# Performance work log

Measured on AMD Instinct MI355X. Metric: run time of the kernel, lower is better.

Reference implementation:

```python
import jax, jax.numpy as jnp
import numpy as np

N, E, F_IN, NUM_GRAPHS, K = 50000, 500000, 160, 128, 3


def _glorot(k, shape):
    lim = np.sqrt(6.0 / (shape[-2] + shape[-1])).astype(np.float32)
    return jax.random.uniform(k, shape, jnp.float32, -lim, lim)


def setup_inputs() -> dict:
    key = jax.random.key(0)
    ks = jax.random.split(key, 8)
    x = jax.random.normal(ks[0], (N, F_IN), jnp.float32)
    edge_index = jax.random.randint(ks[1], (2, E), 0, N)
    edge_attr = jax.random.uniform(ks[2], (E,), jnp.float32)
    batch = jnp.sort(jax.random.randint(ks[3], (N,), 0, NUM_GRAPHS))
    W1 = _glorot(ks[4], (K, F_IN, 128)); b1 = jnp.zeros((128,), jnp.float32)
    W2 = _glorot(ks[5], (K, 128, 64)); b2 = jnp.zeros((64,), jnp.float32)
    W3 = _glorot(ks[6], (K, 64, 32)); b3 = jnp.zeros((32,), jnp.float32)
    Wl = _glorot(ks[7], (32, 2)); bl = jnp.zeros((2,), jnp.float32)
    return dict(x=x, edge_index=edge_index, edge_attr=edge_attr, batch=batch,
                W1=W1, b1=b1, W2=W2, b2=b2, W3=W3, b3=b3, Wl=Wl, bl=bl)


def _cheb_norm(src, dst, edge_attr, n):
    # PyG ChebConv: sym-normalized Laplacian, lambda_max=2 =>
    # L_hat = (2/lmax)*L_sym - I = -D^{-1/2} A D^{-1/2} (diagonal = 0)
    deg = jax.ops.segment_sum(edge_attr, src, num_segments=n)
    safe = jnp.where(deg > 0, deg, 1.0)
    dinv = jnp.where(deg > 0, jax.lax.rsqrt(safe), 0.0)
    return -dinv[src] * edge_attr * dinv[dst]


def _propagate(x, src, dst, w, n):
    # out[dst] += w * x[src]  (sparse L_hat @ x)
    return jax.ops.segment_sum(w[:, None] * x[src], dst, num_segments=n)


def _cheb_conv(x, src, dst, w, W, b, n):
    # Chebyshev recurrence: T0 = x, T1 = L_hat x, Tk = 2 L_hat T(k-1) - T(k-2)
    tx0 = x
    out = tx0 @ W[0]
    tx1 = _propagate(tx0, src, dst, w, n)
    out = out + tx1 @ W[1]
    for k in range(2, W.shape[0]):
        tx2 = 2.0 * _propagate(tx1, src, dst, w, n) - tx0
        out = out + tx2 @ W[k]
        tx0, tx1 = tx1, tx2
    return out + b


def reference(x, edge_index, edge_attr, batch, W1, b1, W2, b2, W3, b3, Wl, bl):
    n = x.shape[0]
    src, dst = edge_index[0], edge_index[1]
    w = _cheb_norm(src, dst, edge_attr, n)
    h = jax.nn.relu(_cheb_conv(x, src, dst, w, W1, b1, n))
    h = jax.nn.relu(_cheb_conv(h, src, dst, w, W2, b2, n))
    h = jax.nn.relu(_cheb_conv(h, src, dst, w, W3, b3, n))
    # global_mean_pool over graph ids (dropout omitted: eval mode)
    sums = jax.ops.segment_sum(h, batch, num_segments=NUM_GRAPHS)
    cnt = jax.ops.segment_sum(jnp.ones((n,), h.dtype), batch, num_segments=NUM_GRAPHS)
    pooled = sums / jnp.maximum(cnt, 1.0)[:, None]
    return pooled @ Wl + bl
```

## Files before the change

kernel.cpp:

```cpp
#include <hip/hip_runtime.h>

#define N_NODES 50000
#define N_EDGES 500000
#define NUM_G   128
#define SCAN_NB 49
#define PN      (SCAN_NB * 1024)
#define HIST_NCX 64
#define HIST_EC  7813
#define HIST_R   16384
#define HIST_NRY 4

typedef __attribute__((ext_vector_type(8))) short short8;
typedef __attribute__((ext_vector_type(4))) float f32x4;

__device__ __forceinline__ unsigned f2bf(float x) {
    unsigned u = __float_as_uint(x);
    return (u + 0x7FFFu + ((u >> 16) & 1u)) >> 16;
}
__device__ __forceinline__ float bf2f(unsigned h) {
    return __uint_as_float(h << 16);
}

__global__ void hist_kernel(const int* __restrict__ src, const int* __restrict__ dst,
                            const float* __restrict__ ea,
                            float* __restrict__ pdeg, int* __restrict__ pcnt) {
    __shared__ unsigned lh[HIST_R];
    int x = blockIdx.x, y = blockIdx.y, tid = threadIdx.x;
    bool isdeg = y < HIST_NRY;
    int base = (isdeg ? y : y - HIST_NRY) * HIST_R;
    for (int i = tid; i < HIST_R; i += 256) lh[i] = 0u;
    __syncthreads();
    int e0 = x * HIST_EC, e1 = min(e0 + HIST_EC, N_EDGES);
    if (isdeg) {
        for (int e = e0 + tid; e < e1; e += 256) {
            int s = src[e];
            if ((unsigned)(s - base) < HIST_R) atomicAdd((float*)&lh[s - base], ea[e]);
        }
    } else {
        for (int e = e0 + tid; e < e1; e += 256) {
            int d = dst[e];
            if ((unsigned)(d - base) < HIST_R) atomicAdd((int*)&lh[d - base], 1);
        }
    }
    __syncthreads();
    if (isdeg) {
        for (int i = tid; i < HIST_R; i += 256) {
            int n = base + i;
            if (n < PN) pdeg[(size_t)x * PN + n] = ((float*)lh)[i];
        }
    } else {
        for (int i = tid; i < HIST_R; i += 256) {
            int n = base + i;
            if (n < PN) pcnt[(size_t)x * PN + n] = ((int*)lh)[i];
        }
    }
}

__global__ void reduce_kernel(const float* __restrict__ pdeg, int* __restrict__ pcnt,
                              float* __restrict__ dinv, int* __restrict__ cnt) {
    int n = blockIdx.x * 256 + threadIdx.x;
    float d = 0.f;
    int run = 0;
    for (int x = 0; x < HIST_NCX; ++x) {
        d += pdeg[(size_t)x * PN + n];
        int v = pcnt[(size_t)x * PN + n];
        pcnt[(size_t)x * PN + n] = run;
        run += v;
    }
    if (n < N_NODES) {
        float r = 0.f;
        if (d > 0.f) {
            r = rsqrtf(d);
            r = r * (1.5f - 0.5f * d * r * r);
        }
        dinv[n] = r;
        cnt[n] = run;
    } else {
        cnt[n] = 0;
    }
}

__global__ void scan_partial_kernel(const int* __restrict__ cnt, int* __restrict__ partial) {
    int b = blockIdx.x, t = threadIdx.x;
    int4 v = reinterpret_cast<const int4*>(cnt)[b * 256 + t];
    int s = v.x + v.y + v.z + v.w;
    __shared__ int red[256];
    red[t] = s;
    __syncthreads();
    for (int off = 128; off > 0; off >>= 1) {
        if (t < off) red[t] += red[t + off];
        __syncthreads();
    }
    if (t == 0) partial[b] = red[0];
}

__global__ void scan_offsets_kernel(int* __restrict__ partial, int* __restrict__ rowptr,
                                    int nb, int n) {
    int t = threadIdx.x;
    int orig = (t < nb) ? partial[t] : 0;
    int v = orig;
    for (int off = 1; off < 64; off <<= 1) {
        int u = __shfl_up(v, off, 64);
        if (t >= off) v += u;
    }
    if (t < nb) partial[t] = v - orig;
    if (t == nb - 1) rowptr[n] = v;
}

__global__ void scan_final_kernel(const int* __restrict__ cnt, const int* __restrict__ partial,
                                  int* __restrict__ rowptr, int n) {
    int b = blockIdx.x, t = threadIdx.x;
    int4 v = reinterpret_cast<const int4*>(cnt)[b * 256 + t];
    int s = v.x + v.y + v.z + v.w;
    __shared__ int red[256];
    red[t] = s;
    __syncthreads();
    for (int off = 1; off < 256; off <<= 1) {
        int u = (t >= off) ? red[t - off] : 0;
        __syncthreads();
        red[t] += u;
        __syncthreads();
    }
    int excl = partial[b] + ((t == 0) ? 0 : red[t - 1]);
    int i0 = b * 1024 + t * 4;
    if (i0 < n)     rowptr[i0]     = excl;
    if (i0 + 1 < n) rowptr[i0 + 1] = excl + v.x;
    if (i0 + 2 < n) rowptr[i0 + 2] = excl + v.x + v.y;
    if (i0 + 3 < n) rowptr[i0 + 3] = excl + v.x + v.y + v.z;
}

__global__ void scatter_kernel(const int* __restrict__ src, const int* __restrict__ dst,
                               const float* __restrict__ ea,
                               const int* __restrict__ rowptr, const int* __restrict__ pcnt,
                               int2* __restrict__ csr) {
    __shared__ int cursor[HIST_R];
    int x = blockIdx.x, y = blockIdx.y, tid = threadIdx.x;
    int base = y * HIST_R;
    for (int i = tid; i < HIST_R; i += 256) {
        int n = base + i;
        cursor[i] = (n < N_NODES) ? (rowptr[n] + pcnt[(size_t)x * PN + n]) : 0;
    }
    __syncthreads();
    int e0 = x * HIST_EC, e1 = min(e0 + HIST_EC, N_EDGES);
    for (int e = e0 + tid; e < e1; e += 256) {
        int d = dst[e];
        if ((unsigned)(d - base) < HIST_R) {
            int pos = atomicAdd(&cursor[d - base], 1);
            int2 ew;
            ew.x = src[e];
            ew.y = __float_as_int(ea[e]);
            csr[pos] = ew;
        }
    }
}

__global__ void conv_bf16_kernel(const float* __restrict__ x, unsigned short* __restrict__ o, int n4) {
    int t = blockIdx.x * blockDim.x + threadIdx.x;
    if (t >= n4) return;
    float4 v = reinterpret_cast<const float4*>(x)[t];
    ushort4 r;
    r.x = (unsigned short)f2bf(v.x);
    r.y = (unsigned short)f2bf(v.y);
    r.z = (unsigned short)f2bf(v.z);
    r.w = (unsigned short)f2bf(v.w);
    *reinterpret_cast<ushort4*>(o + (size_t)t * 4) = r;
}

__device__ __forceinline__ void wprep_one(const float* __restrict__ W, unsigned short* __restrict__ WT,
                                          int t, int FIN, int F) {
    int n = t / FIN, k = t - n * FIN;
    int sel = n / F, c = n - sel * F;
    float v;
    if (sel == 0) v = W[(size_t)k * F + c] - W[(size_t)2 * FIN * F + (size_t)k * F + c];
    else          v = W[(size_t)sel * FIN * F + (size_t)k * F + c];
    WT[t] = (unsigned short)f2bf(v);
}

__global__ void wprep_all_kernel(const float* __restrict__ W1, const float* __restrict__ W2,
                                 const float* __restrict__ W3,
                                 unsigned short* __restrict__ WT1, unsigned short* __restrict__ WT2,
                                 unsigned short* __restrict__ WT3) {
    int t = blockIdx.x * 256 + threadIdx.x;
    if (t < 61440)      wprep_one(W1, WT1, t, 160, 128);
    else if (t < 86016) wprep_one(W2, WT2, t - 61440, 128, 64);
    else if (t < 92160) wprep_one(W3, WT3, t - 86016, 64, 32);
}

template<int FIN, int F>
__launch_bounds__(256)
__global__ void cheb_gemm(const unsigned short* __restrict__ Xb, const unsigned short* __restrict__ WT,
                          const float* __restrict__ dinv,
                          unsigned short* __restrict__ Y0, unsigned short* __restrict__ Y1,
                          unsigned short* __restrict__ Y2,
                          int nrows) {
    constexpr int KT = FIN / 32;
    constexpr int NT = F / 32;
    constexpr int SA = FIN + 8;
    constexpr int F8 = FIN / 8;
    __shared__ short Bs[32 * SA];

    int tid = threadIdx.x;
    int lane = tid & 63, w = tid >> 6;
    int m0 = blockIdx.x * 64;
    int g = blockIdx.y;
    unsigned short* Ys = (g == 0) ? Y0 : (g == 1) ? Y1 : Y2;

    int colb = lane & 15;
    int q8 = (lane >> 4) << 3;
    int rq = (lane >> 4) << 2;
    int arow = m0 + w * 16 + colb;
    bool rok = arow < nrows;

    short8 afr[KT];
    #pragma unroll
    for (int kt = 0; kt < KT; ++kt) {
        short8 z = {0, 0, 0, 0, 0, 0, 0, 0};
        afr[kt] = rok ? *reinterpret_cast<const short8*>(Xb + (size_t)arow * FIN + (kt << 5) + q8) : z;
    }

    for (int nt = 0; nt < NT; ++nt) {
        int n0 = (g * NT + nt) << 5;
        __syncthreads();
        for (int span = tid; span < 32 * F8; span += 256) {
            int r = span / F8, c8 = (span - r * F8) << 3;
            int pr = (r < 16) ? (r << 1) : (((r - 16) << 1) + 1);
            *reinterpret_cast<uint4*>(&Bs[r * SA + c8]) =
                *reinterpret_cast<const uint4*>(WT + (size_t)(n0 + pr) * FIN + c8);
        }
        __syncthreads();

        f32x4 acc0 = {0.f, 0.f, 0.f, 0.f}, acc1 = acc0;
        #pragma unroll
        for (int kt = 0; kt < KT; ++kt) {
            short8 b0 = *reinterpret_cast<const short8*>(&Bs[colb * SA + (kt << 5) + q8]);
            short8 b1 = *reinterpret_cast<const short8*>(&Bs[(colb + 16) * SA + (kt << 5) + q8]);
            acc0 = __builtin_amdgcn_mfma_f32_16x16x32_bf16(afr[kt], b0, acc0, 0, 0, 0);
            acc1 = __builtin_amdgcn_mfma_f32_16x16x32_bf16(afr[kt], b1, acc1, 0, 0, 0);
        }

        int lc = (nt << 5) + (colb << 1);
        #pragma unroll
        for (int r = 0; r < 4; ++r) {
            int orow = m0 + w * 16 + rq + r;
            if (orow < nrows) {
                float sc = (g == 2) ? dinv[orow] : 1.0f;
                unsigned pack = f2bf(acc0[r] * sc) | (f2bf(acc1[r] * sc) << 16);
                *reinterpret_cast<unsigned*>(Ys + (size_t)orow * F + lc) = pack;
            }
        }
    }
}

__device__ __forceinline__ void acc8(float* acc, uint4 p, float wv) {
    acc[0] += wv * bf2f(p.x & 0xFFFFu);
    acc[1] += wv * __uint_as_float(p.x & 0xFFFF0000u);
    acc[2] += wv * bf2f(p.y & 0xFFFFu);
    acc[3] += wv * __uint_as_float(p.y & 0xFFFF0000u);
    acc[4] += wv * bf2f(p.z & 0xFFFFu);
    acc[5] += wv * __uint_as_float(p.z & 0xFFFF0000u);
    acc[6] += wv * bf2f(p.w & 0xFFFFu);
    acc[7] += wv * __uint_as_float(p.w & 0xFFFF0000u);
}

__device__ __forceinline__ void expand8(uint4 p, float* o) {
    o[0] = bf2f(p.x & 0xFFFFu);
    o[1] = __uint_as_float(p.x & 0xFFFF0000u);
    o[2] = bf2f(p.y & 0xFFFFu);
    o[3] = __uint_as_float(p.y & 0xFFFF0000u);
    o[4] = bf2f(p.z & 0xFFFFu);
    o[5] = __uint_as_float(p.z & 0xFFFF0000u);
    o[6] = bf2f(p.w & 0xFFFFu);
    o[7] = __uint_as_float(p.w & 0xFFFF0000u);
}

__global__ void gather_z_kernel(const unsigned short* __restrict__ X, const int2* __restrict__ csr,
                                const int* __restrict__ rowptr, const float* __restrict__ dinv,
                                const unsigned short* __restrict__ Y1, unsigned short* __restrict__ U,
                                int n, int F) {
    int Fq8 = F >> 3;
    int t = blockIdx.x * blockDim.x + threadIdx.x;
    int d = t / Fq8;
    if (d >= n) return;
    int f8 = (t - d * Fq8) << 3;
    int beg = rowptr[d], end = rowptr[d + 1];
    float acc[8] = {0.f, 0.f, 0.f, 0.f, 0.f, 0.f, 0.f, 0.f};
    int i = beg;
    for (; i + 1 < end; i += 2) {
        int2 e0 = csr[i], e1 = csr[i + 1];
        uint4 p0 = *reinterpret_cast<const uint4*>(X + (size_t)e0.x * F + f8);
        uint4 p1 = *reinterpret_cast<const uint4*>(X + (size_t)e1.x * F + f8);
        acc8(acc, p0, __int_as_float(e0.y));
        acc8(acc, p1, __int_as_float(e1.y));
    }
    if (i < end) {
        int2 e0 = csr[i];
        uint4 p0 = *reinterpret_cast<const uint4*>(X + (size_t)e0.x * F + f8);
        acc8(acc, p0, __int_as_float(e0.y));
    }
    float y[8];
    expand8(*reinterpret_cast<const uint4*>(Y1 + (size_t)d * F + f8), y);
    float dv = dinv[d];
    float dv2 = 2.f * dv;
    uint4 o;
    o.x = f2bf(dv * (y[0] - dv2 * acc[0])) | (f2bf(dv * (y[1] - dv2 * acc[1])) << 16);
    o.y = f2bf(dv * (y[2] - dv2 * acc[2])) | (f2bf(dv * (y[3] - dv2 * acc[3])) << 16);
    o.z = f2bf(dv * (y[4] - dv2 * acc[4])) | (f2bf(dv * (y[5] - dv2 * acc[5])) << 16);
    o.w = f2bf(dv * (y[6] - dv2 * acc[6])) | (f2bf(dv * (y[7] - dv2 * acc[7])) << 16);
    *reinterpret_cast<uint4*>(U + (size_t)d * F + f8) = o;
}

__global__ void gather_v_kernel(const unsigned short* __restrict__ X, const int2* __restrict__ csr,
                                const int* __restrict__ rowptr, const float* __restrict__ dinv,
                                const unsigned short* __restrict__ Y0, const float* __restrict__ bias,
                                unsigned short* __restrict__ Xn, int n, int F) {
    int Fq8 = F >> 3;
    int t = blockIdx.x * blockDim.x + threadIdx.x;
    int d = t / Fq8;
    if (d >= n) return;
    int f8 = (t - d * Fq8) << 3;
    int beg = rowptr[d], end = rowptr[d + 1];
    float acc[8] = {0.f, 0.f, 0.f, 0.f, 0.f, 0.f, 0.f, 0.f};
    int i = beg;
    for (; i + 1 < end; i += 2) {
        int2 e0 = csr[i], e1 = csr[i + 1];
        uint4 p0 = *reinterpret_cast<const uint4*>(X + (size_t)e0.x * F + f8);
        uint4 p1 = *reinterpret_cast<const uint4*>(X + (size_t)e1.x * F + f8);
        acc8(acc, p0, __int_as_float(e0.y));
        acc8(acc, p1, __int_as_float(e1.y));
    }
    if (i < end) {
        int2 e0 = csr[i];
        uint4 p0 = *reinterpret_cast<const uint4*>(X + (size_t)e0.x * F + f8);
        acc8(acc, p0, __int_as_float(e0.y));
    }
    float y[8];
    expand8(*reinterpret_cast<const uint4*>(Y0 + (size_t)d * F + f8), y);
    float4 ba = *reinterpret_cast<const float4*>(bias + f8);
    float4 bb = *reinterpret_cast<const float4*>(bias + f8 + 4);
    float dv = dinv[d];
    float v0 = fmaxf(y[0] - dv * acc[0] + ba.x, 0.f);
    float v1 = fmaxf(y[1] - dv * acc[1] + ba.y, 0.f);
    float v2 = fmaxf(y[2] - dv * acc[2] + ba.z, 0.f);
    float v3 = fmaxf(y[3] - dv * acc[3] + ba.w, 0.f);
    float v4 = fmaxf(y[4] - dv * acc[4] + bb.x, 0.f);
    float v5 = fmaxf(y[5] - dv * acc[5] + bb.y, 0.f);
    float v6 = fmaxf(y[6] - dv * acc[6] + bb.z, 0.f);
    float v7 = fmaxf(y[7] - dv * acc[7] + bb.w, 0.f);
    uint4 o;
    o.x = f2bf(v0) | (f2bf(v1) << 16);
    o.y = f2bf(v2) | (f2bf(v3) << 16);
    o.z = f2bf(v4) | (f2bf(v5) << 16);
    o.w = f2bf(v6) | (f2bf(v7) << 16);
    *reinterpret_cast<uint4*>(Xn + (size_t)d * F + f8) = o;
}

__device__ __forceinline__ int lower_bound_dev(const int* __restrict__ a, int n, int v) {
    int lo = 0, hi = n;
    while (lo < hi) {
        int mid = (lo + hi) >> 1;
        if (a[mid] < v) lo = mid + 1; else hi = mid;
    }
    return lo;
}

__global__ void pool_kernel(const unsigned short* __restrict__ H, const int* __restrict__ batch,
                            const float* __restrict__ Wl, const float* __restrict__ bl,
                            float* __restrict__ out, int n) {
    int g = blockIdx.x;
    int start = lower_bound_dev(batch, n, g);
    int end   = lower_bound_dev(batch, n, g + 1);
    int tid = threadIdx.x;
    int f = tid & 31;
    int sub = tid >> 5;
    float acc = 0.0f;
    for (int i = start + sub; i < end; i += 8)
        acc += bf2f((unsigned)H[(size_t)i * 32 + f]);
    __shared__ float red[256];
    red[tid] = acc;
    __syncthreads();
    if (tid < 128) red[tid] += red[tid + 128];
    __syncthreads();
    if (tid < 64) red[tid] += red[tid + 64];
    __syncthreads();
    if (tid < 32) red[tid] += red[tid + 32];
    __syncthreads();
    if (tid < 2) {
        int cnt = end - start;
        float inv = 1.0f / (float)(cnt > 0 ? cnt : 1);
        float o = bl[tid];
        for (int f2 = 0; f2 < 32; ++f2)
            o += red[f2] * inv * Wl[f2 * 2 + tid];
        out[g * 2 + tid] = o;
    }
}

extern "C" void kernel_launch(void* const* d_in, const int* in_sizes, int n_in,
                              void* d_out, int out_size, void* d_ws, size_t ws_size,
                              hipStream_t stream) {
    const float* x     = (const float*)d_in[0];
    const int*   ei    = (const int*)d_in[1];
    const float* ea    = (const float*)d_in[2];
    const int*   batch = (const int*)d_in[3];
    const float* W1 = (const float*)d_in[4];
    const float* b1 = (const float*)d_in[5];
    const float* W2 = (const float*)d_in[6];
    const float* b2 = (const float*)d_in[7];
    const float* W3 = (const float*)d_in[8];
    const float* b3 = (const float*)d_in[9];
    const float* Wl = (const float*)d_in[10];
    const float* bl = (const float*)d_in[11];
    float* out = (float*)d_out;
    char* ws = (char*)d_ws;

    const int* src = ei;
    const int* dst = ei + N_EDGES;

    size_t off = 0;
    auto alloc = [&](size_t bytes) { char* p = ws + off; off += (bytes + 255) & ~(size_t)255; return p; };
    float* pdeg    = (float*)alloc((size_t)HIST_NCX * PN * 4);
    int*   pcnt    = (int*)  alloc((size_t)HIST_NCX * PN * 4);
    float* dinv    = (float*)alloc(N_NODES * 4);
    int*   cnt     = (int*)  alloc((size_t)PN * 4);
    int*   partial = (int*)  alloc(SCAN_NB * 4);
    int*   rowptr  = (int*)  alloc((N_NODES + 1) * 4);
    int2*  csr     = (int2*) alloc((size_t)N_EDGES * 8);
    unsigned short* Xb  = (unsigned short*)alloc((size_t)N_NODES * 160 * 2);
    unsigned short* Y0  = (unsigned short*)alloc((size_t)N_NODES * 128 * 2);
    unsigned short* Y1  = (unsigned short*)alloc((size_t)N_NODES * 128 * 2);
    unsigned short* Y2  = (unsigned short*)alloc((size_t)N_NODES * 128 * 2);
    unsigned short* U   = (unsigned short*)alloc((size_t)N_NODES * 128 * 2);
    unsigned short* WT1 = (unsigned short*)alloc((size_t)384 * 160 * 2);
    unsigned short* WT2 = (unsigned short*)alloc((size_t)192 * 128 * 2);
    unsigned short* WT3 = (unsigned short*)alloc((size_t)96 * 64 * 2);

    const int BT = 256;

    hist_kernel<<<dim3(HIST_NCX, 2 * HIST_NRY), BT, 0, stream>>>(src, dst, ea, pdeg, pcnt);
    reduce_kernel<<<PN / BT, BT, 0, stream>>>(pdeg, pcnt, dinv, cnt);
    scan_partial_kernel<<<SCAN_NB, BT, 0, stream>>>(cnt, partial);
    scan_offsets_kernel<<<1, 64, 0, stream>>>(partial, rowptr, SCAN_NB, N_NODES);
    scan_final_kernel<<<SCAN_NB, BT, 0, stream>>>(cnt, partial, rowptr, N_NODES);
    scatter_kernel<<<dim3(HIST_NCX, HIST_NRY), BT, 0, stream>>>(src, dst, ea, rowptr, pcnt, csr);

    int n4 = N_NODES * 160 / 4;
    conv_bf16_kernel<<<(n4 + BT - 1) / BT, BT, 0, stream>>>(x, Xb, n4);
    wprep_all_kernel<<<360, BT, 0, stream>>>(W1, W2, W3, WT1, WT2, WT3);

    dim3 ggrid((N_NODES + 63) / 64, 3);
    auto gathers = [&](const float* bias, int F) {
        int gth = N_NODES * (F / 8);
        int ggr = (gth + BT - 1) / BT;
        gather_z_kernel<<<ggr, BT, 0, stream>>>(Y2, csr, rowptr, dinv, Y1, U, N_NODES, F);
        gather_v_kernel<<<ggr, BT, 0, stream>>>(U, csr, rowptr, dinv, Y0, bias, Xb, N_NODES, F);
    };

    cheb_gemm<160, 128><<<ggrid, BT, 0, stream>>>(Xb, WT1, dinv, Y0, Y1, Y2, N_NODES);
    gathers(b1, 128);
    cheb_gemm<128, 64><<<ggrid, BT, 0, stream>>>(Xb, WT2, dinv, Y0, Y1, Y2, N_NODES);
    gathers(b2, 64);
    cheb_gemm<64, 32><<<ggrid, BT, 0, stream>>>(Xb, WT3, dinv, Y0, Y1, Y2, N_NODES);
    gathers(b3, 32);

    pool_kernel<<<NUM_G, BT, 0, stream>>>(Xb, batch, Wl, bl, out, N_NODES);
}
```

Measured before the change: 336.9 us.

## Use wavefront-per-node gathers with edge-parallel lanes and fuse preprocessing kernels

Replaces the thread-per-(node, 8-feature chunk) sparse gathers with a templated kernel that assigns one wavefront per destination node. Lanes split the node's edges across slots, prefetch the next CSR entry, and reduce partial sums with xor shuffles. This spreads the work of high-degree nodes across lanes and improves memory-level parallelism, but idles lanes on low-degree nodes and adds shuffle work. It also fuses the degree reduce with the scan partial sums using vectorized loads, and merges the bf16 input conversion with weight prep into one launch, which removes launch overhead.

Result: slower. 416.6 us (+23.7%).

```diff
diff --git a/kernel.cpp b/kernel.cpp
--- a/kernel.cpp
+++ b/kernel.cpp
@@ -9,6 +9,7 @@
 #define HIST_EC  7813
 #define HIST_R   16384
 #define HIST_NRY 4
+#define CONVB    7813
 
 typedef __attribute__((ext_vector_type(8))) short short8;
 typedef __attribute__((ext_vector_type(4))) float f32x4;
@@ -56,34 +57,39 @@
     }
 }
 
-__global__ void reduce_kernel(const float* __restrict__ pdeg, int* __restrict__ pcnt,
-                              float* __restrict__ dinv, int* __restrict__ cnt) {
-    int n = blockIdx.x * 256 + threadIdx.x;
-    float d = 0.f;
-    int run = 0;
+__global__ void reduce_scan_kernel(const float* __restrict__ pdeg, int* __restrict__ pcnt,
+                                   float* __restrict__ dinv, int* __restrict__ cnt,
+                                   int* __restrict__ partial) {
+    int b = blockIdx.x, t = threadIdx.x;
+    int i0 = b * 1024 + t * 4;
+    float d0 = 0.f, d1 = 0.f, d2 = 0.f, d3 = 0.f;
+    int r0 = 0, r1 = 0, r2 = 0, r3 = 0;
     for (int x = 0; x < HIST_NCX; ++x) {
-        d += pdeg[(size_t)x * PN + n];
-        int v = pcnt[(size_t)x * PN + n];
-        pcnt[(size_t)x * PN + n] = run;
-        run += v;
-    }
-    if (n < N_NODES) {
-        float r = 0.f;
-        if (d > 0.f) {
-            r = rsqrtf(d);
-            r = r * (1.5f - 0.5f * d * r * r);
-        }
-        dinv[n] = r;
-        cnt[n] = run;
-    } else {
-        cnt[n] = 0;
-    }
-}
-
-__global__ void scan_partial_kernel(const int* __restrict__ cnt, int* __restrict__ partial) {
-    int b = blockIdx.x, t = threadIdx.x;
-    int4 v = reinterpret_cast<const int4*>(cnt)[b * 256 + t];
-    int s = v.x + v.y + v.z + v.w;
+        float4 pv = *reinterpret_cast<const float4*>(pdeg + (size_t)x * PN + i0);
+        int4   cv = *reinterpret_cast<const int4*>(pcnt + (size_t)x * PN + i0);
+        *reinterpret_cast<int4*>(pcnt + (size_t)x * PN + i0) = make_int4(r0, r1, r2, r3);
+        d0 += pv.x; d1 += pv.y; d2 += pv.z; d3 += pv.w;
+        r0 += cv.x; r1 += cv.y; r2 += cv.z; r3 += cv.w;
+    }
+    float dd[4] = {d0, d1, d2, d3};
+    int   rr[4] = {r0, r1, r2, r3};
+    int s = 0;
+    #pragma unroll
+    for (int j = 0; j < 4; ++j) {
+        int n = i0 + j;
+        if (n < N_NODES) {
+            float dv = dd[j], r = 0.f;
+            if (dv > 0.f) {
+                r = rsqrtf(dv);
+                r = r * (1.5f - 0.5f * dv * r * r);
+            }
+            dinv[n] = r;
+            cnt[n] = rr[j];
+            s += rr[j];
+        } else {
+            cnt[n] = 0;
+        }
+    }
     __shared__ int red[256];
     red[t] = s;
     __syncthreads();
@@ -154,18 +160,6 @@
     }
 }
 
-__global__ void conv_bf16_kernel(const float* __restrict__ x, unsigned short* __restrict__ o, int n4) {
-    int t = blockIdx.x * blockDim.x + threadIdx.x;
-    if (t >= n4) return;
-    float4 v = reinterpret_cast<const float4*>(x)[t];
-    ushort4 r;
-    r.x = (unsigned short)f2bf(v.x);
-    r.y = (unsigned short)f2bf(v.y);
-    r.z = (unsigned short)f2bf(v.z);
-    r.w = (unsigned short)f2bf(v.w);
-    *reinterpret_cast<ushort4*>(o + (size_t)t * 4) = r;
-}
-
 __device__ __forceinline__ void wprep_one(const float* __restrict__ W, unsigned short* __restrict__ WT,
                                           int t, int FIN, int F) {
     int n = t / FIN, k = t - n * FIN;
@@ -176,14 +170,28 @@
     WT[t] = (unsigned short)f2bf(v);
 }
 
-__global__ void wprep_all_kernel(const float* __restrict__ W1, const float* __restrict__ W2,
-                                 const float* __restrict__ W3,
-                                 unsigned short* __restrict__ WT1, unsigned short* __restrict__ WT2,
-                                 unsigned short* __restrict__ WT3) {
-    int t = blockIdx.x * 256 + threadIdx.x;
-    if (t < 61440)      wprep_one(W1, WT1, t, 160, 128);
-    else if (t < 86016) wprep_one(W2, WT2, t - 61440, 128, 64);
-    else if (t < 92160) wprep_one(W3, WT3, t - 86016, 64, 32);
+__global__ void conv_wprep_kernel(const float* __restrict__ x, unsigned short* __restrict__ Xb,
+                                  const float* __restrict__ W1, const float* __restrict__ W2,
+                                  const float* __restrict__ W3,
+                                  unsigned short* __restrict__ WT1, unsigned short* __restrict__ WT2,
+                                  unsigned short* __restrict__ WT3) {
+    int b = blockIdx.x, tid = threadIdx.x;
+    if (b < CONVB) {
+        int t = b * 256 + tid;
+        if (t >= N_NODES * 160 / 4) return;
+        float4 v = reinterpret_cast<const float4*>(x)[t];
+        ushort4 r;
+        r.x = (unsigned short)f2bf(v.x);
+        r.y = (unsigned short)f2bf(v.y);
+        r.z = (unsigned short)f2bf(v.z);
+        r.w = (unsigned short)f2bf(v.w);
+        *reinterpret_cast<ushort4*>(Xb + (size_t)t * 4) = r;
+    } else {
+        int t = (b - CONVB) * 256 + tid;
+        if (t < 61440)      wprep_one(W1, WT1, t, 160, 128);
+        else if (t < 86016) wprep_one(W2, WT2, t - 61440, 128, 64);
+        else if (t < 92160) wprep_one(W3, WT3, t - 86016, 64, 32);
+    }
 }
 
 template<int FIN, int F>
@@ -273,85 +281,68 @@
     o[7] = __uint_as_float(p.w & 0xFFFF0000u);
 }
 
-__global__ void gather_z_kernel(const unsigned short* __restrict__ X, const int2* __restrict__ csr,
-                                const int* __restrict__ rowptr, const float* __restrict__ dinv,
-                                const unsigned short* __restrict__ Y1, unsigned short* __restrict__ U,
-                                int n, int F) {
-    int Fq8 = F >> 3;
-    int t = blockIdx.x * blockDim.x + threadIdx.x;
-    int d = t / Fq8;
-    if (d >= n) return;
-    int f8 = (t - d * Fq8) << 3;
-    int beg = rowptr[d], end = rowptr[d + 1];
+template<int F, int MODE>
+__launch_bounds__(256)
+__global__ void gather_kernel(const unsigned short* __restrict__ X, const int2* __restrict__ csr,
+                              const int* __restrict__ rowptr, const float* __restrict__ dinv,
+                              const unsigned short* __restrict__ Y, const float* __restrict__ bias,
+                              unsigned short* __restrict__ O, int n) {
+    constexpr int FQ8 = F >> 3;
+    constexpr int LF = (F == 128) ? 4 : (F == 64) ? 3 : 2;
+    constexpr int SL = 64 >> LF;
+    int wid = blockIdx.x * 4 + (threadIdx.x >> 6);
+    if (wid >= n) return;
+    int lane = threadIdx.x & 63;
+    int chunk = lane & (FQ8 - 1);
+    int slot = lane >> LF;
+
+    int beg = rowptr[wid];
+    int deg = rowptr[wid + 1] - beg;
     float acc[8] = {0.f, 0.f, 0.f, 0.f, 0.f, 0.f, 0.f, 0.f};
-    int i = beg;
-    for (; i + 1 < end; i += 2) {
-        int2 e0 = csr[i], e1 = csr[i + 1];
-        uint4 p0 = *reinterpret_cast<const uint4*>(X + (size_t)e0.x * F + f8);
-        uint4 p1 = *reinterpret_cast<const uint4*>(X + (size_t)e1.x * F + f8);
-        acc8(acc, p0, __int_as_float(e0.y));
-        acc8(acc, p1, __int_as_float(e1.y));
-    }
-    if (i < end) {
-        int2 e0 = csr[i];
-        uint4 p0 = *reinterpret_cast<const uint4*>(X + (size_t)e0.x * F + f8);
-        acc8(acc, p0, __int_as_float(e0.y));
-    }
-    float y[8];
-    expand8(*reinterpret_cast<const uint4*>(Y1 + (size_t)d * F + f8), y);
-    float dv = dinv[d];
-    float dv2 = 2.f * dv;
-    uint4 o;
-    o.x = f2bf(dv * (y[0] - dv2 * acc[0])) | (f2bf(dv * (y[1] - dv2 * acc[1])) << 16);
-    o.y = f2bf(dv * (y[2] - dv2 * acc[2])) | (f2bf(dv * (y[3] - dv2 * acc[3])) << 16);
-    o.z = f2bf(dv * (y[4] - dv2 * acc[4])) | (f2bf(dv * (y[5] - dv2 * acc[5])) << 16);
-    o.w = f2bf(dv * (y[6] - dv2 * acc[6])) | (f2bf(dv * (y[7] - dv2 * acc[7])) << 16);
-    *reinterpret_cast<uint4*>(U + (size_t)d * F + f8) = o;
-}
-
-__global__ void gather_v_kernel(const unsigned short* __restrict__ X, const int2* __restrict__ csr,
-                                const int* __restrict__ rowptr, const float* __restrict__ dinv,
-                                const unsigned short* __restrict__ Y0, const float* __restrict__ bias,
-                                unsigned short* __restrict__ Xn, int n, int F) {
-    int Fq8 = F >> 3;
-    int t = blockIdx.x * blockDim.x + threadIdx.x;
-    int d = t / Fq8;
-    if (d >= n) return;
-    int f8 = (t - d * Fq8) << 3;
-    int beg = rowptr[d], end = rowptr[d + 1];
-    float acc[8] = {0.f, 0.f, 0.f, 0.f, 0.f, 0.f, 0.f, 0.f};
-    int i = beg;
-    for (; i + 1 < end; i += 2) {
-        int2 e0 = csr[i], e1 = csr[i + 1];
-        uint4 p0 = *reinterpret_cast<const uint4*>(X + (size_t)e0.x * F + f8);
-        uint4 p1 = *reinterpret_cast<const uint4*>(X + (size_t)e1.x * F + f8);
-        acc8(acc, p0, __int_as_float(e0.y));
-        acc8(acc, p1, __int_as_float(e1.y));
-    }
-    if (i < end) {
-        int2 e0 = csr[i];
-        uint4 p0 = *reinterpret_cast<const uint4*>(X + (size_t)e0.x * F + f8);
-        acc8(acc, p0, __int_as_float(e0.y));
-    }
-    float y[8];
-    expand8(*reinterpret_cast<const uint4*>(Y0 + (size_t)d * F + f8), y);
-    float4 ba = *reinterpret_cast<const float4*>(bias + f8);
-    float4 bb = *reinterpret_cast<const float4*>(bias + f8 + 4);
-    float dv = dinv[d];
-    float v0 = fmaxf(y[0] - dv * acc[0] + ba.x, 0.f);
-    float v1 = fmaxf(y[1] - dv * acc[1] + ba.y, 0.f);
-    float v2 = fmaxf(y[2] - dv * acc[2] + ba.z, 0.f);
-    float v3 = fmaxf(y[3] - dv * acc[3] + ba.w, 0.f);
-    float v4 = fmaxf(y[4] - dv * acc[4] + bb.x, 0.f);
-    float v5 = fmaxf(y[5] - dv * acc[5] + bb.y, 0.f);
-    float v6 = fmaxf(y[6] - dv * acc[6] + bb.z, 0.f);
-    float v7 = fmaxf(y[7] - dv * acc[7] + bb.w, 0.f);
-    uint4 o;
-    o.x = f2bf(v0) | (f2bf(v1) << 16);
-    o.y = f2bf(v2) | (f2bf(v3) << 16);
-    o.z = f2bf(v4) | (f2bf(v5) << 16);
-    o.w = f2bf(v6) | (f2bf(v7) << 16);
-    *reinterpret_cast<uint4*>(Xn + (size_t)d * F + f8) = o;
+    int2 e = make_int2(0, 0);
+    if (slot < deg) e = csr[beg + slot];
+    for (int i = slot; i < deg; i += SL) {
+        int nx = i + SL;
+        int2 en = (nx < deg) ? csr[beg + nx] : e;
+        uint4 p = *reinterpret_cast<const uint4*>(X + (size_t)e.x * F + (chunk << 3));
+        acc8(acc, p, __int_as_float(e.y));
+        e = en;
+    }
+    #pragma unroll
+    for (int m = FQ8; m < 64; m <<= 1) {
+        #pragma unroll
+        for (int j = 0; j < 8; ++j)
+            acc[j] += __shfl_xor(acc[j], m, 64);
+    }
+    if (lane < FQ8) {
+        int f8 = lane << 3;
+        float y[8];
+        expand8(*reinterpret_cast<const uint4*>(Y + (size_t)wid * F + f8), y);
+        float dv = dinv[wid];
+        float v[8];
+        if (MODE == 0) {
+            float dv2 = 2.f * dv;
+            #pragma unroll
+            for (int j = 0; j < 8; ++j) v[j] = dv * (y[j] - dv2 * acc[j]);
+        } else {
+            float4 ba = *reinterpret_cast<const float4*>(bias + f8);
+            float4 bb = *reinterpret_cast<const float4*>(bias + f8 + 4);
+            v[0] = fmaxf(y[0] - dv * acc[0] + ba.x, 0.f);
+            v[1] = fmaxf(y[1] - dv * acc[1] + ba.y, 0.f);
+            v[2] = fmaxf(y[2] - dv * acc[2] + ba.z, 0.f);
+            v[3] = fmaxf(y[3] - dv * acc[3] + ba.w, 0.f);
+            v[4] = fmaxf(y[4] - dv * acc[4] + bb.x, 0.f);
+            v[5] = fmaxf(y[5] - dv * acc[5] + bb.y, 0.f);
+            v[6] = fmaxf(y[6] - dv * acc[6] + bb.z, 0.f);
+            v[7] = fmaxf(y[7] - dv * acc[7] + bb.w, 0.f);
+        }
+        uint4 o;
+        o.x = f2bf(v[0]) | (f2bf(v[1]) << 16);
+        o.y = f2bf(v[2]) | (f2bf(v[3]) << 16);
+        o.z = f2bf(v[4]) | (f2bf(v[5]) << 16);
+        o.w = f2bf(v[6]) | (f2bf(v[7]) << 16);
+        *reinterpret_cast<uint4*>(O + (size_t)wid * F + f8) = o;
+    }
 }
 
 __device__ __forceinline__ int lower_bound_dev(const int* __restrict__ a, int n, int v) {
@@ -436,30 +427,26 @@
     const int BT = 256;
 
     hist_kernel<<<dim3(HIST_NCX, 2 * HIST_NRY), BT, 0, stream>>>(src, dst, ea, pdeg, pcnt);
-    reduce_kernel<<<PN / BT, BT, 0, stream>>>(pdeg, pcnt, dinv, cnt);
-    scan_partial_kernel<<<SCAN_NB, BT, 0, stream>>>(cnt, partial);
+    reduce_scan_kernel<<<SCAN_NB, BT, 0, stream>>>(pdeg, pcnt, dinv, cnt, partial);
     scan_offsets_kernel<<<1, 64, 0, stream>>>(partial, rowptr, SCAN_NB, N_NODES);
     scan_final_kernel<<<SCAN_NB, BT, 0, stream>>>(cnt, partial, rowptr, N_NODES);
     scatter_kernel<<<dim3(HIST_NCX, HIST_NRY), BT, 0, stream>>>(src, dst, ea, rowptr, pcnt, csr);
-
-    int n4 = N_NODES * 160 / 4;
-    conv_bf16_kernel<<<(n4 + BT - 1) / BT, BT, 0, stream>>>(x, Xb, n4);
-    wprep_all_kernel<<<360, BT, 0, stream>>>(W1, W2, W3, WT1, WT2, WT3);
+    conv_wprep_kernel<<<CONVB + 360, BT, 0, stream>>>(x, Xb, W1, W2, W3, WT1, WT2, WT3);
 
     dim3 ggrid((N_NODES + 63) / 64, 3);
-    auto gathers = [&](const float* bias, int F) {
-        int gth = N_NODES * (F / 8);
-        int ggr = (gth + BT - 1) / BT;
-        gather_z_kernel<<<ggr, BT, 0, stream>>>(Y2, csr, rowptr, dinv, Y1, U, N_NODES, F);
-        gather_v_kernel<<<ggr, BT, 0, stream>>>(U, csr, rowptr, dinv, Y0, bias, Xb, N_NODES, F);
-    };
+    int gblocks = (N_NODES + 3) / 4;
 
     cheb_gemm<160, 128><<<ggrid, BT, 0, stream>>>(Xb, WT1, dinv, Y0, Y1, Y2, N_NODES);
-    gathers(b1, 128);
+    gather_kernel<128, 0><<<gblocks, BT, 0, stream>>>(Y2, csr, rowptr, dinv, Y1, nullptr, U, N_NODES);
+    gather_kernel<128, 1><<<gblocks, BT, 0, stream>>>(U, csr, rowptr, dinv, Y0, b1, Xb, N_NODES);
+
     cheb_gemm<128, 64><<<ggrid, BT, 0, stream>>>(Xb, WT2, dinv, Y0, Y1, Y2, N_NODES);
-    gathers(b2, 64);
+    gather_kernel<64, 0><<<gblocks, BT, 0, stream>>>(Y2, csr, rowptr, dinv, Y1, nullptr, U, N_NODES);
+    gather_kernel<64, 1><<<gblocks, BT, 0, stream>>>(U, csr, rowptr, dinv, Y0, b2, Xb, N_NODES);
+
     cheb_gemm<64, 32><<<ggrid, BT, 0, stream>>>(Xb, WT3, dinv, Y0, Y1, Y2, N_NODES);
-    gathers(b3, 32);
+    gather_kernel<32, 0><<<gblocks, BT, 0, stream>>>(Y2, csr, rowptr, dinv, Y1, nullptr, U, N_NODES);
+    gather_kernel<32, 1><<<gblocks, BT, 0, stream>>>(U, csr, rowptr, dinv, Y0, b3, Xb, N_NODES);
 
     pool_kernel<<<NUM_G, BT, 0, stream>>>(Xb, batch, Wl, bl, out, N_NODES);
 }
```
